# Optimization experiments

Hardware: AMD Instinct MI355X
Metric: run time of the kernel (lower is better)

The kernel has to match this reference:

```python
import jax, jax.numpy as jnp
import numpy as np

B, S, D = 4, 4096, 768  # batch, seq_len, n_units
NEG = -1000000000.0      # masked_fill value from the torch source


def setup_inputs() -> dict:
    key = jax.random.key(0)
    ks = jax.random.split(key, 12)
    scale = 1.0 / np.sqrt(D)
    inp = {
        "query": jax.random.normal(ks[0], (B, S, D), jnp.float32),
        "key_": jax.random.normal(ks[1], (B, S, D), jnp.float32),
        "value": jax.random.normal(ks[2], (B, S, D), jnp.float32),
        # nn.Linear weights are [out, in]; forward computes x @ W.T + b
        "Wq": jax.random.normal(ks[3], (D, D), jnp.float32) * scale,
        "bq": jnp.zeros((D,), jnp.float32),
        "Wk": jax.random.normal(ks[4], (D, D), jnp.float32) * scale,
        "bk": jnp.zeros((D,), jnp.float32),
        "Wv": jax.random.normal(ks[5], (D, D), jnp.float32) * scale,
        "bv": jnp.zeros((D,), jnp.float32),
        "Wo": jax.random.normal(ks[6], (D, D), jnp.float32) * scale,
        "bo": jnp.zeros((D,), jnp.float32),
        # broadcastable causal mask [1, S, S]; 0 -> masked
        "mask": jnp.tril(jnp.ones((S, S), jnp.int32))[None, :, :],
    }
    return inp


def reference(query, key_, value, Wq, bq, Wk, bk, Wv, bv, Wo, bo, mask):
    # QKV projections (torch Linear: x @ W.T + b)
    q = jnp.einsum("bsd,ed->bse", query, Wq) + bq
    k = jnp.einsum("bsd,ed->bse", key_, Wk) + bk
    v = jnp.einsum("bsd,ed->bse", value, Wv) + bv
    # scores: NOTE source scales by n_units**0.5 (full model dim, no head split)
    weights = jnp.einsum("bqd,bkd->bqk", q, k) / jnp.sqrt(jnp.float32(D))
    weights = jnp.where(mask == 0, jnp.float32(NEG), weights)
    weights = jax.nn.softmax(weights, axis=-1)
    # dropout is identity in eval/deterministic reference
    attended = jnp.einsum("bqk,bkd->bqd", weights, v)
    return jnp.einsum("bsd,ed->bse", attended, Wo) + bo
```

## Files before the change

kernel.cpp:

```cpp
#include <hip/hip_runtime.h>
#include <hip/hip_bf16.h>
#include <stdint.h>

#define DI __device__ __forceinline__

typedef __bf16 bf16x4 __attribute__((ext_vector_type(4)));
typedef __bf16 bf16x8 __attribute__((ext_vector_type(8)));
typedef float  f32x4  __attribute__((ext_vector_type(4)));

static constexpr int  BATCH = 4;
static constexpr int  SEQ   = 4096;
static constexpr int  DIM   = 768;
static constexpr long TOK   = (long)BATCH * SEQ;
static constexpr int  QT    = SEQ / 128;
static constexpr int  NTRI  = QT * (QT + 1) / 2;
static constexpr float SCALE = 0.0360843918243516150f;

__global__ void cvt3_kernel(const float* __restrict__ a, const float* __restrict__ b,
                            const float* __restrict__ c, __bf16* __restrict__ oa,
                            __bf16* __restrict__ ob, __bf16* __restrict__ oc, long n4){
  const float* in  = blockIdx.y == 0 ? a : blockIdx.y == 1 ? b : c;
  __bf16*      out = blockIdx.y == 0 ? oa : blockIdx.y == 1 ? ob : oc;
  long i = (long)blockIdx.x * blockDim.x + threadIdx.x;
  const long stride = (long)gridDim.x * blockDim.x;
  for(; i < n4; i += stride){
    float4 v = ((const float4*)in)[i];
    bf16x4 o = { (__bf16)v.x, (__bf16)v.y, (__bf16)v.z, (__bf16)v.w };
    ((bf16x4*)out)[i] = o;
  }
}
__global__ void cvt4_kernel(const float* __restrict__ a, const float* __restrict__ b,
                            const float* __restrict__ c, const float* __restrict__ d,
                            __bf16* __restrict__ oa, __bf16* __restrict__ ob,
                            __bf16* __restrict__ oc, __bf16* __restrict__ od, long n4){
  const float* in  = blockIdx.y == 0 ? a : blockIdx.y == 1 ? b : blockIdx.y == 2 ? c : d;
  __bf16*      out = blockIdx.y == 0 ? oa : blockIdx.y == 1 ? ob : blockIdx.y == 2 ? oc : od;
  long i = (long)blockIdx.x * blockDim.x + threadIdx.x;
  const long stride = (long)gridDim.x * blockDim.x;
  for(; i < n4; i += stride){
    float4 v = ((const float4*)in)[i];
    bf16x4 o = { (__bf16)v.x, (__bf16)v.y, (__bf16)v.z, (__bf16)v.w };
    ((bf16x4*)out)[i] = o;
  }
}

DI int swz_off(int r, int c){ return (r << 7) + ((c ^ (r & 7)) << 4); }

template<int NT, int R>
DI void stage(const __bf16* __restrict__ src, long ld, char* lds, int tid){
  const int w = tid >> 6, l = tid & 63;
  const int rsub = l >> 3;
  const int kc   = (l & 7) ^ rsub;
  const __bf16* g = src + (long)(w * 8 + rsub) * ld + kc * 8;
  char* d = lds + (w << 10);
  constexpr int RPC = NT / 8;
  #pragma unroll
  for(int i = 0; i < R / RPC; ++i){
    __builtin_amdgcn_global_load_lds(
        (const __attribute__((address_space(1))) void*)(g + (long)(i * RPC) * ld),
        (__attribute__((address_space(3))) void*)(d + i * RPC * 128), 16, 0, 0);
  }
}

template<int NT, int R>
DI void stage_add(const __bf16* __restrict__ a0, const __bf16* __restrict__ a1,
                  long ld, char* lds, int tid){
  const int w = tid >> 6, l = tid & 63;
  const int rsub = l >> 3;
  const int kc   = (l & 7) ^ rsub;
  const long off = (long)(w * 8 + rsub) * ld + kc * 8;
  char* d = lds + (w << 10) + (l << 4);
  constexpr int RPC = NT / 8;
  #pragma unroll
  for(int i = 0; i < R / RPC; ++i){
    bf16x8 v0 = *(const bf16x8*)(a0 + off + (long)(i * RPC) * ld);
    bf16x8 v1 = *(const bf16x8*)(a1 + off + (long)(i * RPC) * ld);
    bf16x8 o;
    #pragma unroll
    for(int e = 0; e < 8; ++e) o[e] = (__bf16)((float)v0[e] + (float)v1[e]);
    *(bf16x8*)(d + i * RPC * 128) = o;
  }
}

DI bf16x8 frag_ld(const char* lds, int row, int c){
  return *(const bf16x8*)(lds + swz_off(row, c));
}

DI void mma_tile(const char* As, const char* Bs, int lane, int wr, int wc, f32x4 acc[4][4]){
  #pragma unroll
  for(int kk = 0; kk < 2; ++kk){
    const int c = kk * 4 + (lane >> 4);
    bf16x8 a[4], b[4];
    #pragma unroll
    for(int i = 0; i < 4; ++i) a[i] = frag_ld(As, wr + i * 16 + (lane & 15), c);
    #pragma unroll
    for(int j = 0; j < 4; ++j) b[j] = frag_ld(Bs, wc + j * 16 + (lane & 15), c);
    #pragma unroll
    for(int i = 0; i < 4; ++i)
      #pragma unroll
      for(int j = 0; j < 4; ++j)
        acc[i][j] = __builtin_amdgcn_mfma_f32_16x16x32_bf16(a[i], b[j], acc[i][j], 0, 0, 0);
  }
}

template<class FA, class FB>
DI void kloop2(FA fa, long lda, FB fb, long ldb, int nt, int tid,
               char* As, char* Bs, f32x4 acc[4][4]){
  const int lane = tid & 63, w = tid >> 6;
  const int wr = (w >> 2) * 64, wc = (w & 3) * 64;
  for(int t = 0; t < nt; ++t){
    stage<512, 128>(fa(t), lda, As, tid);
    stage<512, 256>(fb(t), ldb, Bs, tid);
    __syncthreads();
    mma_tile(As, Bs, lane, wr, wc, acc);
    __syncthreads();
  }
}

DI void issue_unit(const __bf16* __restrict__ src, long ld, char* slab, int tid){
  const int w = tid >> 6, lane = tid & 63;
  #pragma unroll
  for(int r = 0; r < 2; ++r){
    const int row = w * 16 + (lane >> 2) + r * 128;
    const int c   = (lane & 3) ^ ((row >> 1) & 3);
    const __bf16* g = src + (long)row * ld + c * 8;
    __builtin_amdgcn_global_load_lds(
        (const __attribute__((address_space(1))) void*)g,
        (__attribute__((address_space(3))) void*)(slab + w * 1024 + r * 8192), 16, 0, 0);
  }
}

template<int G>
DI void mma16(f32x4 (&acc)[8][4], const bf16x8 (&a)[4], const bf16x8 (&b)[4]){
  __builtin_amdgcn_s_setprio(1);
  #pragma unroll
  for(int i = 0; i < 4; ++i)
    #pragma unroll
    for(int j = 0; j < 4; ++j)
      acc[G * 4 + i][j] =
          __builtin_amdgcn_mfma_f32_16x16x32_bf16(a[i], b[j], acc[G * 4 + i][j], 0, 0, 0);
  __builtin_amdgcn_s_setprio(0);
}
template<int G>
DI void rdA(bf16x8 (&a)[4], const char* LA, int sbase, const int (&offA)[8]){
  #pragma unroll
  for(int i = 0; i < 4; ++i) a[i] = *(const bf16x8*)(LA + sbase + offA[G * 4 + i]);
}
DI void rdB(bf16x8 (&b)[4], const char* LB, int sbase, const int (&offB)[4]){
  #pragma unroll
  for(int j = 0; j < 4; ++j) b[j] = *(const bf16x8*)(LB + sbase + offB[j]);
}
#define VMW(N) asm volatile("s_waitcnt vmcnt(" #N ")" ::: "memory")

template<class FA, class FB>
DI void kloop8(FA fa, long lda, FB fb, long ldb, int nt, int tid,
               char* L, f32x4 (&acc)[8][4]){
  const int lane = tid & 63, w = tid >> 6;
  int offA[8], offB[4];
  #pragma unroll
  for(int i = 0; i < 8; ++i){
    const int r = (w >> 2) * 128 + i * 16 + (lane & 15);
    offA[i] = r * 64 + ((((lane >> 4)) ^ ((r >> 1) & 3)) << 4);
  }
  #pragma unroll
  for(int j = 0; j < 4; ++j){
    const int r = (w & 3) * 64 + j * 16 + (lane & 15);
    offB[j] = r * 64 + ((((lane >> 4)) ^ ((r >> 1) & 3)) << 4);
  }
  char* LA = L;
  char* LB = L + 65536;
  auto AS = [](int s, int k){ return s * 32768 + k * 16384; };
  issue_unit(fa(0),      lda, LA + AS(0, 0), tid);
  issue_unit(fb(0),      ldb, LB + AS(0, 0), tid);
  issue_unit(fa(0) + 32, lda, LA + AS(0, 1), tid);
  issue_unit(fb(0) + 32, ldb, LB + AS(0, 1), tid);
  issue_unit(fa(1),      lda, LA + AS(1, 0), tid);
  issue_unit(fb(1),      ldb, LB + AS(1, 0), tid);
  bf16x8 a[4], b[4];
  for(int t = 0; t < nt; t += 2){
    const bool more = (t + 2 < nt);
    VMW(8); __builtin_amdgcn_s_barrier();
    issue_unit(fa(t + 1) + 32, lda, LA + AS(1, 1), tid);
    rdB(b, LB, AS(0, 0), offB);
    rdA<0>(a, LA, AS(0, 0), offA);  mma16<0>(acc, a, b);
    issue_unit(fb(t + 1) + 32, ldb, LB + AS(1, 1), tid);
    rdA<1>(a, LA, AS(0, 0), offA);  mma16<1>(acc, a, b);
    VMW(8); __builtin_amdgcn_s_barrier();
    if(more) issue_unit(fa(t + 2), lda, LA + AS(0, 0), tid);
    rdB(b, LB, AS(0, 1), offB);
    rdA<0>(a, LA, AS(0, 1), offA);  mma16<0>(acc, a, b);
    if(more) issue_unit(fb(t + 2), ldb, LB + AS(0, 0), tid);
    rdA<1>(a, LA, AS(0, 1), offA);  mma16<1>(acc, a, b);
    if(more){ VMW(8); } else { VMW(4); }
    __builtin_amdgcn_s_barrier();
    if(more) issue_unit(fa(t + 2) + 32, lda, LA + AS(0, 1), tid);
    rdB(b, LB, AS(1, 0), offB);
    rdA<0>(a, LA, AS(1, 0), offA);  mma16<0>(acc, a, b);
    if(more) issue_unit(fb(t + 2) + 32, ldb, LB + AS(0, 1), tid);
    rdA<1>(a, LA, AS(1, 0), offA);  mma16<1>(acc, a, b);
    if(more){ VMW(8); } else { VMW(0); }
    __builtin_amdgcn_s_barrier();
    if(more) issue_unit(fa(t + 3), lda, LA + AS(1, 0), tid);
    rdB(b, LB, AS(1, 1), offB);
    rdA<0>(a, LA, AS(1, 1), offA);  mma16<0>(acc, a, b);
    if(more) issue_unit(fb(t + 3), ldb, LB + AS(1, 0), tid);
    rdA<1>(a, LA, AS(1, 1), offA);  mma16<1>(acc, a, b);
  }
}

DI int xcd_swz(int bid, int n){ const int c = n >> 3; return (bid & 7) * c + (bid >> 3); }

__global__ __launch_bounds__(512, 2)
void proj_qkv(const __bf16* __restrict__ xq, const __bf16* __restrict__ xk,
              const __bf16* __restrict__ xv, const __bf16* __restrict__ Wqb,
              const __bf16* __restrict__ Wkb, const __bf16* __restrict__ Wvb,
              const float* __restrict__ bq, const float* __restrict__ bk,
              const float* __restrict__ bv, __bf16* __restrict__ qb,
              __bf16* __restrict__ kb, __bf16* __restrict__ vbT){
  __shared__ __attribute__((aligned(128))) char L[131072];
  const int z = blockIdx.y, tid = threadIdx.x;
  const int bid = xcd_swz(blockIdx.x, 192);
  const __bf16 *A, *B; const float* bias; __bf16* C;
  long m0, n0, ldc; bool biasm;
  if(z == 0){ A = xq;  B = Wqb; bias = bq; C = qb;
              m0 = (long)(bid / 3) * 256; n0 = (bid % 3) * 256; ldc = DIM; biasm = false; }
  else if(z == 1){ A = xk;  B = Wkb; bias = bk; C = kb;
              m0 = (long)(bid / 3) * 256; n0 = (bid % 3) * 256; ldc = DIM; biasm = false; }
  else {      A = Wvb; B = xv;  bias = bv; C = vbT;
              m0 = (long)(bid / 64) * 256; n0 = (bid % 64) * 256; ldc = TOK; biasm = true; }
  const __bf16* Ar = A + m0 * DIM;
  const __bf16* Br = B + n0 * DIM;
  f32x4 acc[8][4] = {};
  auto fa = [&](int t){ return Ar + t * 64; };
  auto fb = [&](int t){ return Br + t * 64; };
  kloop8(fa, DIM, fb, DIM, DIM / 64, tid, L, acc);

  const int lane = tid & 63, w = tid >> 6;
  const int cl = lane & 15, rq = (lane >> 4) * 4;
  #pragma unroll
  for(int i = 0; i < 8; ++i)
    #pragma unroll
    for(int j = 0; j < 4; ++j){
      const long gc = n0 + (w & 3) * 64 + j * 16 + cl;
      #pragma unroll
      for(int e = 0; e < 4; ++e){
        const long gr = m0 + (w >> 2) * 128 + i * 16 + rq + e;
        C[gr * ldc + gc] = (__bf16)(acc[i][j][e] + bias[biasm ? gr : gc]);
      }
    }
}

__global__ __launch_bounds__(512)
void qk_kernel(const __bf16* __restrict__ qb, const __bf16* __restrict__ kb,
               __bf16* __restrict__ Pc, float* __restrict__ rlsum){
  const int sid = xcd_swz(blockIdx.x, 1088);
  const int b = sid / 272, t2 = sid % 272, tid = threadIdx.x;
  int Qi = (int)((sqrtf(4.0f * t2 + 1.0f) - 1.0f) * 0.5f);
  while((Qi + 1) * (Qi + 2) <= t2) Qi++;
  while(Qi * (Qi + 1) > t2) Qi--;
  const int ki = t2 - Qi * (Qi + 1);
  const __bf16* Aq = qb + ((long)b * SEQ + Qi * 256) * DIM;
  const __bf16* Bk = kb + ((long)b * SEQ + ki * 128) * DIM;
  __shared__ __attribute__((aligned(128))) char As[32768];
  __shared__ __attribute__((aligned(128))) char Bs[16384];
  const int lane = tid & 63, w = tid >> 6;
  const int wr = (w >> 1) * 64, wc = (w & 1) * 64;
  f32x4 acc[4][4] = {};
  for(int t = 0; t < DIM / 64; ++t){
    stage<512, 256>(Aq + t * 64, DIM, As, tid);
    stage<512, 128>(Bk + t * 64, DIM, Bs, tid);
    __syncthreads();
    mma_tile(As, Bs, lane, wr, wc, acc);
    __syncthreads();
  }
  const int cl = lane & 15, rq = (lane >> 4) * 4;
  #pragma unroll
  for(int i = 0; i < 4; ++i){
    const int rbase = wr + i * 16;
    const int qi = 2 * Qi + (rbase >> 7);
    if(ki > qi) continue;
    const bool diag = (ki == qi);
    __bf16* tile = Pc + ((long)b * NTRI + (long)qi * (qi + 1) / 2 + ki) * 16384;
    float rsum[4] = {0.f, 0.f, 0.f, 0.f};
    #pragma unroll
    for(int j = 0; j < 4; ++j){
      const int c = wc + j * 16 + cl;
      #pragma unroll
      for(int e = 0; e < 4; ++e){
        const int rloc = (rbase + rq + e) & 127;
        float p = (diag && c > rloc) ? 0.0f
                  : __expf(fminf(acc[i][j][e] * SCALE, 30.0f));
        tile[rloc * 128 + c] = (__bf16)p;
        rsum[e] += p;
      }
    }
    #pragma unroll
    for(int e = 0; e < 4; ++e){
      float s = rsum[e];
      s += __shfl_xor(s, 1); s += __shfl_xor(s, 2);
      s += __shfl_xor(s, 4); s += __shfl_xor(s, 8);
      if(cl == 0){
        const long gr = (long)b * SEQ + Qi * 256 + rbase + rq + e;
        atomicAdd(&rlsum[gr], s);
      }
    }
  }
}

__global__ __launch_bounds__(512)
void pv_kernel(const __bf16* __restrict__ Pc, const float* __restrict__ rlsum,
               const __bf16* __restrict__ vbT, __bf16* __restrict__ att0,
               __bf16* __restrict__ att1){
  __shared__ __attribute__((aligned(128))) char As[16384];
  __shared__ __attribute__((aligned(128))) char Bs[32768];
  __shared__ float sRl[128];
  const int x = blockIdx.x, y = blockIdx.y, tid = threadIdx.x;
  const long n0 = (long)(x >> 2) * 256;
  const int b = x & 3;
  int qi, k0, k1, half;
  if(y == 62){ qi = 0; k0 = 0; k1 = 1; half = 0; }
  else{
    qi = 31 - (y >> 1); half = y & 1;
    const int c0 = (qi + 2) >> 1;
    if(half == 0){ k0 = 0; k1 = c0; } else { k0 = c0; k1 = qi + 1; }
  }
  if(tid < 128) sRl[tid] = 1.0f / rlsum[b * SEQ + qi * 128 + tid];
  const __bf16* Pq = Pc + ((long)b * NTRI + (long)qi * (qi + 1) / 2) * 16384;
  const __bf16* Bv = vbT + n0 * TOK + (long)b * SEQ;
  f32x4 acc[4][4] = {};
  auto fa = [&](int t){ return Pq + (long)(k0 + (t >> 1)) * 16384 + (t & 1) * 64; };
  auto fb = [&](int t){ return Bv + (long)k0 * 128 + t * 64; };
  kloop2(fa, 128, fb, TOK, 2 * (k1 - k0), tid, As, Bs, acc);

  __bf16* dst = half ? att1 : att0;
  const int lane = tid & 63, w = tid >> 6;
  const int wr = (w >> 2) * 64, wc = (w & 3) * 64;
  const int cl = lane & 15, rq = (lane >> 4) * 4;
  #pragma unroll
  for(int i = 0; i < 4; ++i)
    #pragma unroll
    for(int j = 0; j < 4; ++j){
      const long gc = n0 + wc + j * 16 + cl;
      #pragma unroll
      for(int e = 0; e < 4; ++e){
        const int rloc = wr + i * 16 + rq + e;
        float v = acc[i][j][e] * sRl[rloc];
        dst[((long)b * SEQ + qi * 128 + rloc) * DIM + gc] = (__bf16)v;
      }
    }
  if(y == 62){
    const int r = tid >> 2;
    const int c0 = (tid & 3) * 64;
    __bf16* z0 = att1 + ((long)b * SEQ + r) * DIM + n0 + c0;
    bf16x8 zz = {};
    #pragma unroll
    for(int i = 0; i < 8; ++i) *(bf16x8*)(z0 + i * 8) = zz;
  }
}

__global__ __launch_bounds__(512)
void oproj(const __bf16* __restrict__ att0, const __bf16* __restrict__ att1,
           const __bf16* __restrict__ Wob, const float* __restrict__ bo,
           float* __restrict__ out){
  __shared__ __attribute__((aligned(128))) char As[16384];
  __shared__ __attribute__((aligned(128))) char Bs[32768];
  const int bid = blockIdx.x, tid = threadIdx.x;
  const long n0 = (bid % 3) * 256, m0 = (long)(bid / 3) * 128;
  const __bf16* Br = Wob + n0 * DIM;
  f32x4 acc[4][4] = {};
  const int lane = tid & 63, w = tid >> 6;
  const int wr = (w >> 2) * 64, wc = (w & 3) * 64;
  for(int t = 0; t < DIM / 64; ++t){
    stage_add<512, 128>(att0 + m0 * DIM + t * 64, att1 + m0 * DIM + t * 64, DIM, As, tid);
    stage<512, 256>(Br + t * 64, DIM, Bs, tid);
    __syncthreads();
    mma_tile(As, Bs, lane, wr, wc, acc);
    __syncthreads();
  }
  const int cl = lane & 15, rq = (lane >> 4) * 4;
  #pragma unroll
  for(int i = 0; i < 4; ++i)
    #pragma unroll
    for(int j = 0; j < 4; ++j){
      const long gc = n0 + wc + j * 16 + cl;
      #pragma unroll
      for(int e = 0; e < 4; ++e){
        const long gr = m0 + wr + i * 16 + rq + e;
        out[gr * DIM + gc] = acc[i][j][e] + bo[gc];
      }
    }
}

extern "C" void kernel_launch(void* const* d_in, const int* in_sizes, int n_in,
                              void* d_out, int out_size, void* d_ws, size_t ws_size,
                              hipStream_t stream){
  const float* query = (const float*)d_in[0];
  const float* key_  = (const float*)d_in[1];
  const float* value = (const float*)d_in[2];
  const float* Wq = (const float*)d_in[3];
  const float* bq = (const float*)d_in[4];
  const float* Wk = (const float*)d_in[5];
  const float* bk = (const float*)d_in[6];
  const float* Wv = (const float*)d_in[7];
  const float* bv = (const float*)d_in[8];
  const float* Wo = (const float*)d_in[9];
  const float* bo = (const float*)d_in[10];

  char* p = (char*)d_ws;
  auto carve = [&](size_t bytes)->char*{
    char* r = p; p += (bytes + 255) & ~(size_t)255; return r;
  };
  const size_t tb = (size_t)TOK * DIM * 2;
  __bf16* xq  = (__bf16*)carve(tb);
  __bf16* xk  = (__bf16*)carve(tb);
  __bf16* xv  = (__bf16*)carve(tb);
  __bf16* qb  = (__bf16*)carve(tb);
  __bf16* kb  = (__bf16*)carve(tb);
  __bf16* vbT = (__bf16*)carve(tb);
  __bf16* Wqb = (__bf16*)carve((size_t)DIM * DIM * 2);
  __bf16* Wkb = (__bf16*)carve((size_t)DIM * DIM * 2);
  __bf16* Wvb = (__bf16*)carve((size_t)DIM * DIM * 2);
  __bf16* Wob = (__bf16*)carve((size_t)DIM * DIM * 2);
  __bf16* Pc  = (__bf16*)carve((size_t)BATCH * NTRI * 16384 * 2);
  float*  rlr = (float*)carve((size_t)TOK * 4);
  __bf16* att0 = xq;
  __bf16* att1 = xk;
  if((size_t)(p - (char*)d_ws) > ws_size) return;

  const long nIn4 = TOK * DIM / 4, nW4 = (long)DIM * DIM / 4;
  dim3 g3(2048, 3), g4((unsigned)((nW4 + 255) / 256), 4);
  hipMemsetAsync(rlr, 0, (size_t)TOK * 4, stream);
  cvt3_kernel<<<g3, 256, 0, stream>>>(query, key_, value, xq, xk, xv, nIn4);
  cvt4_kernel<<<g4, 256, 0, stream>>>(Wq, Wk, Wv, Wo, Wqb, Wkb, Wvb, Wob, nW4);

  proj_qkv<<<dim3(192, 3), 512, 0, stream>>>(xq, xk, xv, Wqb, Wkb, Wvb,
                                             bq, bk, bv, qb, kb, vbT);

  qk_kernel<<<1088, 512, 0, stream>>>(qb, kb, Pc, rlr);

  pv_kernel<<<dim3(12, 63), 512, 0, stream>>>(Pc, rlr, vbT, att0, att1);

  oproj<<<384, 512, 0, stream>>>(att0, att1, Wob, bo, (float*)d_out);
}
```

Before: 286.3 us.

## Split PV key range into up to three chunks and merge cvt kernels

```diff
diff --git a/kernel.cpp b/kernel.cpp
--- a/kernel.cpp
+++ b/kernel.cpp
@@ -16,25 +16,25 @@
 static constexpr int  NTRI  = QT * (QT + 1) / 2;
 static constexpr float SCALE = 0.0360843918243516150f;
 
-__global__ void cvt3_kernel(const float* __restrict__ a, const float* __restrict__ b,
-                            const float* __restrict__ c, __bf16* __restrict__ oa,
-                            __bf16* __restrict__ ob, __bf16* __restrict__ oc, long n4){
-  const float* in  = blockIdx.y == 0 ? a : blockIdx.y == 1 ? b : c;
-  __bf16*      out = blockIdx.y == 0 ? oa : blockIdx.y == 1 ? ob : oc;
-  long i = (long)blockIdx.x * blockDim.x + threadIdx.x;
-  const long stride = (long)gridDim.x * blockDim.x;
-  for(; i < n4; i += stride){
-    float4 v = ((const float4*)in)[i];
-    bf16x4 o = { (__bf16)v.x, (__bf16)v.y, (__bf16)v.z, (__bf16)v.w };
-    ((bf16x4*)out)[i] = o;
-  }
-}
-__global__ void cvt4_kernel(const float* __restrict__ a, const float* __restrict__ b,
-                            const float* __restrict__ c, const float* __restrict__ d,
-                            __bf16* __restrict__ oa, __bf16* __restrict__ ob,
-                            __bf16* __restrict__ oc, __bf16* __restrict__ od, long n4){
-  const float* in  = blockIdx.y == 0 ? a : blockIdx.y == 1 ? b : blockIdx.y == 2 ? c : d;
-  __bf16*      out = blockIdx.y == 0 ? oa : blockIdx.y == 1 ? ob : blockIdx.y == 2 ? oc : od;
+__global__ void cvt_all(const float* __restrict__ a0, const float* __restrict__ a1,
+                        const float* __restrict__ a2, const float* __restrict__ a3,
+                        const float* __restrict__ a4, const float* __restrict__ a5,
+                        const float* __restrict__ a6,
+                        __bf16* __restrict__ o0, __bf16* __restrict__ o1,
+                        __bf16* __restrict__ o2, __bf16* __restrict__ o3,
+                        __bf16* __restrict__ o4, __bf16* __restrict__ o5,
+                        __bf16* __restrict__ o6, long n4big, long n4w){
+  const int y = blockIdx.y;
+  const float* in; __bf16* out; long n4;
+  switch(y){
+    case 0: in = a0; out = o0; n4 = n4big; break;
+    case 1: in = a1; out = o1; n4 = n4big; break;
+    case 2: in = a2; out = o2; n4 = n4big; break;
+    case 3: in = a3; out = o3; n4 = n4w;   break;
+    case 4: in = a4; out = o4; n4 = n4w;   break;
+    case 5: in = a5; out = o5; n4 = n4w;   break;
+    default: in = a6; out = o6; n4 = n4w;  break;
+  }
   long i = (long)blockIdx.x * blockDim.x + threadIdx.x;
   const long stride = (long)gridDim.x * blockDim.x;
   for(; i < n4; i += stride){
@@ -63,8 +63,8 @@
 }
 
 template<int NT, int R>
-DI void stage_add(const __bf16* __restrict__ a0, const __bf16* __restrict__ a1,
-                  long ld, char* lds, int tid){
+DI void stage_add3(const __bf16* __restrict__ a0, const __bf16* __restrict__ a1,
+                   const __bf16* __restrict__ a2, long ld, char* lds, int tid){
   const int w = tid >> 6, l = tid & 63;
   const int rsub = l >> 3;
   const int kc   = (l & 7) ^ rsub;
@@ -75,9 +75,11 @@
   for(int i = 0; i < R / RPC; ++i){
     bf16x8 v0 = *(const bf16x8*)(a0 + off + (long)(i * RPC) * ld);
     bf16x8 v1 = *(const bf16x8*)(a1 + off + (long)(i * RPC) * ld);
+    bf16x8 v2 = *(const bf16x8*)(a2 + off + (long)(i * RPC) * ld);
     bf16x8 o;
     #pragma unroll
-    for(int e = 0; e < 8; ++e) o[e] = (__bf16)((float)v0[e] + (float)v1[e]);
+    for(int e = 0; e < 8; ++e)
+      o[e] = (__bf16)((float)v0[e] + (float)v1[e] + (float)v2[e]);
     *(bf16x8*)(d + i * RPC * 128) = o;
   }
 }
@@ -310,29 +312,29 @@
 __global__ __launch_bounds__(512)
 void pv_kernel(const __bf16* __restrict__ Pc, const float* __restrict__ rlsum,
                const __bf16* __restrict__ vbT, __bf16* __restrict__ att0,
-               __bf16* __restrict__ att1){
+               __bf16* __restrict__ att1, __bf16* __restrict__ att2){
   __shared__ __attribute__((aligned(128))) char As[16384];
   __shared__ __attribute__((aligned(128))) char Bs[32768];
   __shared__ float sRl[128];
   const int x = blockIdx.x, y = blockIdx.y, tid = threadIdx.x;
   const long n0 = (long)(x >> 2) * 256;
   const int b = x & 3;
-  int qi, k0, k1, half;
-  if(y == 62){ qi = 0; k0 = 0; k1 = 1; half = 0; }
-  else{
-    qi = 31 - (y >> 1); half = y & 1;
-    const int c0 = (qi + 2) >> 1;
-    if(half == 0){ k0 = 0; k1 = c0; } else { k0 = c0; k1 = qi + 1; }
-  }
+  int qi, ch, nch;
+  if(y < 30){ qi = 31 - y / 3; ch = y % 3; nch = 3; }
+  else if(y < 52){ qi = 21 - (y - 30) / 2; ch = (y - 30) & 1; nch = 2; }
+  else { qi = 10 - (y - 52); ch = 0; nch = 1; }
+  const int ntile = qi + 1, base = ntile / nch, rem = ntile % nch;
+  const int k0 = ch * base + (ch < rem ? ch : rem);
+  const int sz = base + (ch < rem ? 1 : 0);
   if(tid < 128) sRl[tid] = 1.0f / rlsum[b * SEQ + qi * 128 + tid];
   const __bf16* Pq = Pc + ((long)b * NTRI + (long)qi * (qi + 1) / 2) * 16384;
   const __bf16* Bv = vbT + n0 * TOK + (long)b * SEQ;
   f32x4 acc[4][4] = {};
   auto fa = [&](int t){ return Pq + (long)(k0 + (t >> 1)) * 16384 + (t & 1) * 64; };
   auto fb = [&](int t){ return Bv + (long)k0 * 128 + t * 64; };
-  kloop2(fa, 128, fb, TOK, 2 * (k1 - k0), tid, As, Bs, acc);
-
-  __bf16* dst = half ? att1 : att0;
+  kloop2(fa, 128, fb, TOK, 2 * sz, tid, As, Bs, acc);
+
+  __bf16* dst = ch == 0 ? att0 : (ch == 1 ? att1 : att2);
   const int lane = tid & 63, w = tid >> 6;
   const int wr = (w >> 2) * 64, wc = (w & 3) * 64;
   const int cl = lane & 15, rq = (lane >> 4) * 4;
@@ -348,20 +350,24 @@
         dst[((long)b * SEQ + qi * 128 + rloc) * DIM + gc] = (__bf16)v;
       }
     }
-  if(y == 62){
+  if(ch == 0 && nch < 3){
     const int r = tid >> 2;
     const int c0 = (tid & 3) * 64;
-    __bf16* z0 = att1 + ((long)b * SEQ + r) * DIM + n0 + c0;
+    const long rowoff = ((long)b * SEQ + qi * 128 + r) * DIM + n0 + c0;
     bf16x8 zz = {};
     #pragma unroll
-    for(int i = 0; i < 8; ++i) *(bf16x8*)(z0 + i * 8) = zz;
+    for(int i = 0; i < 8; ++i) *(bf16x8*)(att2 + rowoff + i * 8) = zz;
+    if(nch < 2){
+      #pragma unroll
+      for(int i = 0; i < 8; ++i) *(bf16x8*)(att1 + rowoff + i * 8) = zz;
+    }
   }
 }
 
 __global__ __launch_bounds__(512)
 void oproj(const __bf16* __restrict__ att0, const __bf16* __restrict__ att1,
-           const __bf16* __restrict__ Wob, const float* __restrict__ bo,
-           float* __restrict__ out){
+           const __bf16* __restrict__ att2, const __bf16* __restrict__ Wob,
+           const float* __restrict__ bo, float* __restrict__ out){
   __shared__ __attribute__((aligned(128))) char As[16384];
   __shared__ __attribute__((aligned(128))) char Bs[32768];
   const int bid = blockIdx.x, tid = threadIdx.x;
@@ -371,7 +377,8 @@
   const int lane = tid & 63, w = tid >> 6;
   const int wr = (w >> 2) * 64, wc = (w & 3) * 64;
   for(int t = 0; t < DIM / 64; ++t){
-    stage_add<512, 128>(att0 + m0 * DIM + t * 64, att1 + m0 * DIM + t * 64, DIM, As, tid);
+    stage_add3<512, 128>(att0 + m0 * DIM + t * 64, att1 + m0 * DIM + t * 64,
+                         att2 + m0 * DIM + t * 64, DIM, As, tid);
     stage<512, 256>(Br + t * 64, DIM, Bs, tid);
     __syncthreads();
     mma_tile(As, Bs, lane, wr, wc, acc);
@@ -425,20 +432,21 @@
   float*  rlr = (float*)carve((size_t)TOK * 4);
   __bf16* att0 = xq;
   __bf16* att1 = xk;
+  __bf16* att2 = xv;
   if((size_t)(p - (char*)d_ws) > ws_size) return;
 
   const long nIn4 = TOK * DIM / 4, nW4 = (long)DIM * DIM / 4;
-  dim3 g3(2048, 3), g4((unsigned)((nW4 + 255) / 256), 4);
   hipMemsetAsync(rlr, 0, (size_t)TOK * 4, stream);
-  cvt3_kernel<<<g3, 256, 0, stream>>>(query, key_, value, xq, xk, xv, nIn4);
-  cvt4_kernel<<<g4, 256, 0, stream>>>(Wq, Wk, Wv, Wo, Wqb, Wkb, Wvb, Wob, nW4);
+  cvt_all<<<dim3(2048, 7), 256, 0, stream>>>(query, key_, value, Wq, Wk, Wv, Wo,
+                                             xq, xk, xv, Wqb, Wkb, Wvb, Wob,
+                                             nIn4, nW4);
 
   proj_qkv<<<dim3(192, 3), 512, 0, stream>>>(xq, xk, xv, Wqb, Wkb, Wvb,
                                              bq, bk, bv, qb, kb, vbT);
 
   qk_kernel<<<1088, 512, 0, stream>>>(qb, kb, Pc, rlr);
 
-  pv_kernel<<<dim3(12, 63), 512, 0, stream>>>(Pc, rlr, vbT, att0, att1);
-
-  oproj<<<384, 512, 0, stream>>>(att0, att1, Wob, bo, (float*)d_out);
-}
+  pv_kernel<<<dim3(12, 63), 512, 0, stream>>>(Pc, rlr, vbT, att0, att1, att2);
+
+  oproj<<<384, 512, 0, stream>>>(att0, att1, att2, Wob, bo, (float*)d_out);
+}
```

Result: slower. 313.0 us (+9.3%).
